# Kernel tuning notes

Hardware: AMD Instinct MI355X
Metric: run time of the kernel (lower is better)

## Reference

```python
import jax, jax.numpy as jnp
import numpy as np

H = 16  # num_heads


def setup_inputs() -> dict:
    key = jax.random.key(0)
    ks = jax.random.split(key, 12)
    B, T, D, E = 2, 2048, 1024, 16384
    s = 0.02
    return {
        "x": jax.random.normal(ks[0], (B, T, D), jnp.float32),
        "Wq": jax.random.normal(ks[1], (D, D), jnp.float32) * s,
        "bq": jnp.zeros((D,), jnp.float32),
        "Wk": jax.random.normal(ks[2], (D, D), jnp.float32) * s,
        "bk": jnp.zeros((D,), jnp.float32),
        "Wv": jax.random.normal(ks[3], (D, D), jnp.float32) * s,
        "bv": jnp.zeros((D,), jnp.float32),
        "Wo": jax.random.normal(ks[4], (D, D), jnp.float32) * s,
        "bo": jnp.zeros((D,), jnp.float32),
        "edge_emb": jax.random.normal(ks[5], (3, D), jnp.float32) * s,  # TypedEdgeEmbedding table
        "type_w": jax.random.normal(ks[6], (D,), jnp.float32) * s,      # type_to_bias Linear(D,1,bias=False)
        "edge_src": jax.random.randint(ks[7], (E,), 0, T, jnp.int32),
        "edge_dst": jax.random.randint(ks[8], (E,), 0, T, jnp.int32),
        "edge_types": jax.random.randint(ks[9], (E,), 0, 3, jnp.int32),
    }


def reference(x, Wq, bq, Wk, bk, Wv, bv, Wo, bo, edge_emb, type_w,
              edge_src, edge_dst, edge_types):
    B, T, D = x.shape
    hd = D // H
    scale = 1.0 / jnp.sqrt(jnp.float32(hd))
    # QKV projections -> [B, H, T, hd]
    q = (x @ Wq + bq).reshape(B, T, H, hd).transpose(0, 2, 1, 3)
    k = (x @ Wk + bk).reshape(B, T, H, hd).transpose(0, 2, 1, 3)
    v = (x @ Wv + bv).reshape(B, T, H, hd).transpose(0, 2, 1, 3)
    # dense attention scores [B, H, T, T]
    scores = jnp.einsum('bhqd,bhkd->bhqk', q, k) * scale
    # typed edge bias: emb lookup -> linear to scalar per edge; same across B, H
    bias_e = edge_emb[edge_types] @ type_w  # [E]
    # scatter-add bias into scores at (src, dst) for every batch/head
    scores = scores.at[:, :, edge_src, edge_dst].add(bias_e)
    attn = jax.nn.softmax(scores, axis=-1)  # dropout is identity in eval / p=0
    out = jnp.einsum('bhqk,bhkd->bhqd', attn, v)
    out = out.transpose(0, 2, 1, 3).reshape(B, T, D)
    return out @ Wo + bo
```

## Files before the change

### kernel.cpp

```cpp
#include <hip/hip_runtime.h>


typedef __attribute__((ext_vector_type(4))) float f32x4;
typedef __attribute__((ext_vector_type(16))) float f32x16;
typedef __bf16 bf16x8 __attribute__((ext_vector_type(8)));

#define DEV static __device__ __forceinline__

DEV ushort f2bf(float f) {
  unsigned u = __float_as_uint(f);
  unsigned r = u + 0x7fffu + ((u >> 16) & 1u);
  return (ushort)(r >> 16);
}

DEV float bf2f(ushort u) { return __uint_as_float((unsigned)u << 16); }

DEV void gl_lds16(const void* g, void* l) {
  __builtin_amdgcn_global_load_lds(
      (const __attribute__((address_space(1))) void*)g,
      (__attribute__((address_space(3))) void*)l, 16, 0, 0);
}

DEV f32x16 mfma32(bf16x8 a, bf16x8 b, f32x16 c) {
  return __builtin_amdgcn_mfma_f32_32x32x16_bf16(a, b, c, 0, 0, 0);
}

DEV unsigned cvtpk(float a, float b) {
  unsigned r;
  asm("v_cvt_pk_bf16_f32 %0, %1, %2" : "=v"(r) : "v"(a), "v"(b));
  return r;
}

__global__ __launch_bounds__(256) void tcvt5_kernel(
    const float* __restrict__ W0, const float* __restrict__ W1,
    const float* __restrict__ W2, const float* __restrict__ W3,
    ushort* __restrict__ Wt, const float* __restrict__ X,
    ushort* __restrict__ Y) {
  const int z = blockIdx.z;
  if (z == 4) {
    const int lb = blockIdx.y * 32 + blockIdx.x;
#pragma unroll
    for (int j = 0; j < 4; ++j) {
      const int i = lb * 1024 + j * 256 + threadIdx.x;
      float4 v = ((const float4*)X)[i];
      ushort4 o;
      o.x = f2bf(v.x); o.y = f2bf(v.y); o.z = f2bf(v.z); o.w = f2bf(v.w);
      ((ushort4*)Y)[i] = o;
    }
    return;
  }
  __shared__ float tile[32][33];
  const float* W = (z == 0) ? W0 : (z == 1) ? W1 : (z == 2) ? W2 : W3;
  ushort* dst = Wt + (size_t)z * 1048576;
  int bx = blockIdx.x * 32, by = blockIdx.y * 32;
  int tx = threadIdx.x & 31, ty = threadIdx.x >> 5;
#pragma unroll
  for (int i = 0; i < 32; i += 8)
    tile[ty + i][tx] = W[(size_t)(by + ty + i) * 1024 + bx + tx];
  __syncthreads();
#pragma unroll
  for (int i = 0; i < 32; i += 8)
    dst[(size_t)(bx + ty + i) * 1024 + by + tx] = f2bf(tile[tx][ty + i]);
}

__global__ __launch_bounds__(256) void zeroE_kernel(
    const int* __restrict__ src, const int* __restrict__ dst,
    float* __restrict__ BiasT, int E) {
  int e = blockIdx.x * 256 + threadIdx.x;
  if (e < E) BiasT[(size_t)dst[e] * 2048 + src[e]] = 0.0f;
}

__global__ __launch_bounds__(256) void scatterT2_kernel(
    const int* __restrict__ src, const int* __restrict__ dst,
    const int* __restrict__ typ, const float* __restrict__ emb,
    const float* __restrict__ tw, float* __restrict__ BiasT, int E) {
  __shared__ float red[256][3];
  const int t = threadIdx.x;
  float p0 = 0.f, p1 = 0.f, p2 = 0.f;
  for (int d = t; d < 1024; d += 256) {
    const float w = tw[d];
    p0 += emb[d] * w;
    p1 += emb[1024 + d] * w;
    p2 += emb[2048 + d] * w;
  }
  red[t][0] = p0; red[t][1] = p1; red[t][2] = p2;
  __syncthreads();
  for (int s = 128; s > 0; s >>= 1) {
    if (t < s) {
      red[t][0] += red[t + s][0];
      red[t][1] += red[t + s][1];
      red[t][2] += red[t + s][2];
    }
    __syncthreads();
  }
  int e = blockIdx.x * 256 + t;
  if (e < E) {
    const float b = red[0][typ[e]];
    atomicAdd(&BiasT[(size_t)dst[e] * 2048 + src[e]], b);
  }
}

__global__ __launch_bounds__(256) void dexpE_kernel(
    const int* __restrict__ src, const int* __restrict__ dst,
    const float* __restrict__ BiasT, ushort* __restrict__ DT4, int E) {
  int e = blockIdx.x * 256 + threadIdx.x;
  if (e < E) {
    const int k = dst[e], q = src[e];
    const float b = BiasT[(size_t)k * 2048 + q];
    DT4[((size_t)(k >> 2) * 2048 + q) * 4 + (k & 3)] = f2bf(__expf(b) - 1.0f);
  }
}

__global__ __launch_bounds__(512, 4) void gemm_qkv_kernel(
    const ushort* __restrict__ A, const ushort* __restrict__ Bt3,
    const float* __restrict__ bq, const float* __restrict__ bk,
    const float* __restrict__ bv, ushort* __restrict__ Qo,
    ushort* __restrict__ Ko, ushort* __restrict__ Vt2) {
  __shared__ alignas(16) char Als[2][16384];
  __shared__ alignas(16) char Bls[2][16384];
  const int tid = threadIdx.x, w = tid >> 6, l = tid & 63;
  const int m0 = blockIdx.y * 128, n0 = blockIdx.x * 128;
  const int sr = l >> 2, sg = l & 3;
  const int c = l & 15, gg = l >> 4;
  const int wr = (w >> 1) * 32, wc = (w & 1) * 64;

  f32x4 acc[2][4];
  const f32x4 zf = {0.f, 0.f, 0.f, 0.f};
#pragma unroll
  for (int a2 = 0; a2 < 2; ++a2)
#pragma unroll
    for (int b2 = 0; b2 < 4; ++b2) acc[a2][b2] = zf;

  auto STAGE = [&](int buf, int k0) {
#pragma unroll
    for (int j = 0; j < 2; ++j) {
      const int idx = w * 2 + j, kk = idx >> 3, mb = idx & 7;
      gl_lds16(A + (size_t)(m0 + mb * 16 + sr) * 1024 + k0 + kk * 32 + sg * 8,
               &Als[buf][idx * 1024]);
      gl_lds16(Bt3 + (size_t)(n0 + mb * 16 + sr) * 1024 + k0 + kk * 32 + sg * 8,
               &Bls[buf][idx * 1024]);
    }
  };

  STAGE(0, 0);
  STAGE(1, 64);
  for (int t = 0; t < 16; ++t) {
    const int cur = t & 1;
    if (t < 15) asm volatile("s_waitcnt vmcnt(4)" ::: "memory");
    else        asm volatile("s_waitcnt vmcnt(0)" ::: "memory");
    __builtin_amdgcn_s_barrier();

    bf16x8 af[2][2], bfr[2][4];
#pragma unroll
    for (int kk = 0; kk < 2; ++kk) {
#pragma unroll
      for (int f = 0; f < 2; ++f)
        af[kk][f] = *(const bf16x8*)&Als[cur][(kk * 8 + (wr >> 4) + f) * 1024 + c * 64 + gg * 16];
#pragma unroll
      for (int f = 0; f < 4; ++f)
        bfr[kk][f] = *(const bf16x8*)&Bls[cur][(kk * 8 + (wc >> 4) + f) * 1024 + c * 64 + gg * 16];
    }
    asm volatile("s_waitcnt lgkmcnt(0)" ::: "memory");
    __builtin_amdgcn_sched_barrier(0);
    __builtin_amdgcn_s_barrier();

    if (t < 14) STAGE(cur, (t + 2) * 64);

#pragma unroll
    for (int kk = 0; kk < 2; ++kk)
#pragma unroll
      for (int mf = 0; mf < 2; ++mf)
#pragma unroll
        for (int nf = 0; nf < 4; ++nf)
          acc[mf][nf] = __builtin_amdgcn_mfma_f32_16x16x32_bf16(
              af[kk][mf], bfr[kk][nf], acc[mf][nf], 0, 0, 0);
  }

  const int which = n0 >> 10;
  const float scale = (which == 0) ? 0.125f : 1.0f;
  const float* bias = (which == 0) ? bq : (which == 1) ? bk : bv;
#pragma unroll
  for (int mf = 0; mf < 2; ++mf) {
#pragma unroll
    for (int nf = 0; nf < 4; ++nf) {
      const int coln = (n0 & 1023) + wc + nf * 16 + c;
      const float bvv = bias[coln];
      const int h = coln >> 6, d = coln & 63;
#pragma unroll
      for (int i = 0; i < 4; ++i) {
        const int row = m0 + wr + mf * 16 + gg * 4 + i;
        const int b = row >> 11, t = row & 2047;
        const float v = (acc[mf][nf][i] + bvv) * scale;
        const ushort bfv = f2bf(v);
        if (which == 0)
          Qo[((size_t)(b * 16 + h) * 2048 + t) * 64 + d] = bfv;
        else if (which == 1)
          Ko[((size_t)(b * 16 + h) * 2048 + t) * 64 + d] = bfv;
        else
          Vt2[(((size_t)(b * 16 + h) * 32 + (t >> 6)) * 64 + d) * 64 + (t & 63)] = bfv;
      }
    }
  }
}

__global__ __launch_bounds__(256) void gemm_out_kernel(
    const ushort* __restrict__ A, const ushort* __restrict__ Bt,
    const float* __restrict__ bias, float* __restrict__ outp) {
  __shared__ alignas(16) char Als[8192];
  __shared__ alignas(16) char Bls[16384];
  const int tid = threadIdx.x, w = tid >> 6, l = tid & 63;
  const int lin = blockIdx.x;
  const int swz = (lin & 7) * 64 + (lin >> 3);
  const int m0 = (swz >> 3) * 64, n0 = (swz & 7) * 128;
  const int sr = l >> 2, sg = l & 3;
  const int c = l & 15, gg = l >> 4;
  const int wr = (w & 1) * 32, wc = (w >> 1) * 64;

  f32x4 acc[2][4];
  const f32x4 zf = {0.f, 0.f, 0.f, 0.f};
#pragma unroll
  for (int a2 = 0; a2 < 2; ++a2)
#pragma unroll
    for (int b2 = 0; b2 < 4; ++b2) acc[a2][b2] = zf;

  for (int k0 = 0; k0 < 1024; k0 += 64) {
#pragma unroll
    for (int j = 0; j < 2; ++j) {
      const int idx = w * 2 + j, kk = idx >> 2, mb = idx & 3;
      gl_lds16(A + (size_t)(m0 + mb * 16 + sr) * 1024 + k0 + kk * 32 + sg * 8,
               &Als[idx * 1024]);
    }
#pragma unroll
    for (int j = 0; j < 4; ++j) {
      const int idx = w * 4 + j, kk = idx >> 3, mb = idx & 7;
      gl_lds16(Bt + (size_t)(n0 + mb * 16 + sr) * 1024 + k0 + kk * 32 + sg * 8,
               &Bls[idx * 1024]);
    }
    __syncthreads();
#pragma unroll
    for (int kk = 0; kk < 2; ++kk) {
      bf16x8 af[2], bfr[4];
#pragma unroll
      for (int f = 0; f < 2; ++f)
        af[f] = *(const bf16x8*)&Als[(kk * 4 + (wr >> 4) + f) * 1024 + c * 64 + gg * 16];
#pragma unroll
      for (int f = 0; f < 4; ++f)
        bfr[f] = *(const bf16x8*)&Bls[(kk * 8 + (wc >> 4) + f) * 1024 + c * 64 + gg * 16];
#pragma unroll
      for (int mf = 0; mf < 2; ++mf)
#pragma unroll
        for (int nf = 0; nf < 4; ++nf)
          acc[mf][nf] = __builtin_amdgcn_mfma_f32_16x16x32_bf16(
              af[mf], bfr[nf], acc[mf][nf], 0, 0, 0);
    }
    __syncthreads();
  }

#pragma unroll
  for (int mf = 0; mf < 2; ++mf) {
#pragma unroll
    for (int nf = 0; nf < 4; ++nf) {
      const int col = n0 + wc + nf * 16 + c;
      const float bvv = bias[col];
#pragma unroll
      for (int i = 0; i < 4; ++i) {
        const int row = m0 + wr + mf * 16 + gg * 4 + i;
        outp[(size_t)row * 1024 + col] = acc[mf][nf][i] + bvv;
      }
    }
  }
}

__global__ __launch_bounds__(512, 4) void attn12_kernel(
    const ushort* __restrict__ Q, const ushort* __restrict__ K,
    const ushort* __restrict__ Vt2, const ushort* __restrict__ DT4,
    ushort* __restrict__ Out) {
  __shared__ alignas(16) char smem[65536];
  const int tid = threadIdx.x, w = tid >> 6, l = tid & 63;
  const int c = l & 31, hi = l >> 5;
  const int bid = blockIdx.x;
  const int bh = (bid & 7) * 4 + ((bid >> 3) & 3);
  const int qt = bid >> 5;
  const int bI = bh >> 4, h = bh & 15;
  const int qd = w >> 2, ww = w & 3;
  const int qw = qt * 128 + ww * 32;
  const int kq = qd * 1024;
  const int qsb = qd * 32768;
  const char* Kg = (const char*)(K + (size_t)bh * 2048 * 64);
  const char* Vg = (const char*)(Vt2 + (size_t)bh * 32 * 64 * 64);

  const ushort* Qp = Q + ((size_t)bh * 2048 + qw + c) * 64 + hi * 8;
  bf16x8 Qf[4];
#pragma unroll
  for (int ds = 0; ds < 4; ++ds) Qf[ds] = *(const bf16x8*)(Qp + ds * 16);

  const int srb = ww * 8 + (l >> 3);
  const int scol = ((l & 7) << 4) ^ ((l >> 3) << 4);
  const int cx = (c & 7) << 4;

  const ushort* Dbase = DT4 + ((size_t)(kq >> 2) * 2048 + qw + c) * 4;

  f32x16 oacc0 = {0,0,0,0,0,0,0,0,0,0,0,0,0,0,0,0};
  f32x16 oacc1 = {0,0,0,0,0,0,0,0,0,0,0,0,0,0,0,0};
  float l_run = 0.f;

  auto STAGE = [&](int buf, int t0) {
#pragma unroll
    for (int j = 0; j < 2; ++j) {
      const int r = j * 32 + srb;
      gl_lds16(Kg + (size_t)(kq + t0 + r) * 128 + scol,
               &smem[qsb + buf * 8192 + j * 4096 + ww * 1024]);
      gl_lds16(Vg + ((size_t)((kq + t0) >> 6) * 64 + r) * 128 + scol,
               &smem[qsb + 16384 + buf * 8192 + j * 4096 + ww * 1024]);
    }
  };

  STAGE(0, 0);
  for (int t = 0; t < 16; ++t) {
    const int cur = t & 1;
    __syncthreads();
    if (t < 15) STAGE(cur ^ 1, (t + 1) * 64);
    const char* KsC = smem + qsb + cur * 8192;
    const char* VsC = smem + qsb + 16384 + cur * 8192;

    f32x16 s0 = {0,0,0,0,0,0,0,0,0,0,0,0,0,0,0,0};
    f32x16 s1 = {0,0,0,0,0,0,0,0,0,0,0,0,0,0,0,0};
#pragma unroll
    for (int ds = 0; ds < 4; ++ds) {
      const int col = (ds * 32 + hi * 16) ^ cx;
      bf16x8 k0 = *(const bf16x8*)(KsC + c * 128 + col);
      bf16x8 k1 = *(const bf16x8*)(KsC + (32 + c) * 128 + col);
      s0 = mfma32(k0, Qf[ds], s0);
      s1 = mfma32(k1, Qf[ds], s1);
    }

    const ushort* dp = Dbase + (size_t)t * 16 * 8192;
    ushort4 dreg[8];
#pragma unroll
    for (int g = 0; g < 4; ++g) {
      dreg[g]     = *(const ushort4*)(dp + (size_t)(2 * g + hi) * 8192);
      dreg[4 + g] = *(const ushort4*)(dp + (size_t)(8 + 2 * g + hi) * 8192);
    }

    float ps[16];
#pragma unroll
    for (int r = 0; r < 16; ++r) {
      const float d0 = bf2f(((const ushort*)&dreg[r >> 2])[r & 3]);
      const float d1 = bf2f(((const ushort*)&dreg[4 + (r >> 2)])[r & 3]);
      float p0 = __expf(s0[r] - 3.0f);
      float p1 = __expf(s1[r] - 3.0f);
      p0 = fmaf(p0, d0, p0);
      p1 = fmaf(p1, d1, p1);
      s0[r] = p0; s1[r] = p1;
      ps[r] = p0 + p1;
    }
#pragma unroll
    for (int off = 8; off; off >>= 1)
#pragma unroll
      for (int r = 0; r < off; ++r) ps[r] += ps[r + off];
    l_run += ps[0];

    bf16x8 paf[2][2];
#pragma unroll
    for (int kt = 0; kt < 2; ++kt) {
      const f32x16& sv = kt ? s1 : s0;
#pragma unroll
      for (int sl = 0; sl < 2; ++sl) {
        const int rb = sl * 8;
        unsigned u0 = cvtpk(sv[rb + 0], sv[rb + 1]);
        unsigned u1 = cvtpk(sv[rb + 2], sv[rb + 3]);
        unsigned u2 = cvtpk(sv[rb + 4], sv[rb + 5]);
        unsigned u3 = cvtpk(sv[rb + 6], sv[rb + 7]);
        asm("v_permlane32_swap_b32 %0, %1" : "+v"(u0), "+v"(u2));
        asm("v_permlane32_swap_b32 %0, %1" : "+v"(u1), "+v"(u3));
        uint4 uu = {u0, u1, u2, u3};
        paf[kt][sl] = *(bf16x8*)&uu;
      }
    }

#pragma unroll
    for (int kt = 0; kt < 2; ++kt)
#pragma unroll
      for (int sl = 0; sl < 2; ++sl) {
        const int ks = kt * 2 + sl;
        const int col = (ks * 32 + hi * 16) ^ cx;
        bf16x8 v0 = *(const bf16x8*)(VsC + c * 128 + col);
        bf16x8 v1 = *(const bf16x8*)(VsC + (32 + c) * 128 + col);
        oacc0 = mfma32(paf[kt][sl], v0, oacc0);
        oacc1 = mfma32(paf[kt][sl], v1, oacc1);
      }
  }

  __syncthreads();
  const float l_tot = l_run + __shfl_xor(l_run, 32);
  float* mb  = (float*)smem + ww * 2048;
  float* lb  = (float*)(smem + 32768);
  float* lb2 = (float*)(smem + 32768 + 512);
  if (qd == 1) {
#pragma unroll
    for (int r = 0; r < 16; ++r) {
      const int qr = (r & 3) + 8 * (r >> 2) + 4 * hi;
      mb[qr * 64 + c] = oacc0[r];
      mb[qr * 64 + 32 + c] = oacc1[r];
    }
    lb[ww * 32 + c] = l_tot;
  }
  __syncthreads();
  if (qd == 0) {
    const float linv = 1.0f / (l_tot + lb[ww * 32 + c]);
    lb2[ww * 32 + c] = linv;
    const float* lp = lb2 + ww * 32 + hi * 4;
    f32x4 lv[4];
#pragma unroll
    for (int g2 = 0; g2 < 4; ++g2) lv[g2] = *(const f32x4*)(lp + 8 * g2);
    ushort* Ob = Out + ((size_t)bI * 2048 + qw) * 1024 + h * 64;
#pragma unroll
    for (int r = 0; r < 16; ++r) {
      const int qr = (r & 3) + 8 * (r >> 2) + 4 * hi;
      const float sc = lv[r >> 2][r & 3];
      const float o0 = (oacc0[r] + mb[qr * 64 + c]) * sc;
      const float o1 = (oacc1[r] + mb[qr * 64 + 32 + c]) * sc;
      Ob[(size_t)qr * 1024 + c] = f2bf(o0);
      Ob[(size_t)qr * 1024 + 32 + c] = f2bf(o1);
    }
  }
}

extern "C" void kernel_launch(void* const* d_in, const int* in_sizes, int n_in,
                              void* d_out, int out_size, void* d_ws, size_t ws_size,
                              hipStream_t stream) {
  (void)n_in; (void)out_size; (void)ws_size;
  const float* x   = (const float*)d_in[0];
  const float* Wq  = (const float*)d_in[1];
  const float* bq  = (const float*)d_in[2];
  const float* Wk  = (const float*)d_in[3];
  const float* bk  = (const float*)d_in[4];
  const float* Wv  = (const float*)d_in[5];
  const float* bv  = (const float*)d_in[6];
  const float* Wo  = (const float*)d_in[7];
  const float* bo  = (const float*)d_in[8];
  const float* emb = (const float*)d_in[9];
  const float* tw  = (const float*)d_in[10];
  const int* esrc  = (const int*)d_in[11];
  const int* edst  = (const int*)d_in[12];
  const int* etyp  = (const int*)d_in[13];
  const int E = in_sizes[11];

  char* ws = (char*)d_ws;
  const size_t MB = 1u << 20;
  ushort* Wtq = (ushort*)(ws + 0 * MB);
  ushort* Wto = (ushort*)(ws + 6 * MB);
  ushort* Wt3 = Wtq;
  ushort* Qb  = (ushort*)(ws + 8 * MB);
  ushort* Kb  = (ushort*)(ws + 16 * MB);
  ushort* Vt2 = (ushort*)(ws + 24 * MB);
  ushort* Ab  = (ushort*)(ws + 32 * MB);
  float*  BiasT = (float*)(ws + 40 * MB);
  ushort* xbf = (ushort*)d_out;
  ushort* DT4 = (ushort*)((char*)d_out + 8388608);

  const int eb = (E + 255) / 256;
  dim3 tg(32, 32, 5);
  tcvt5_kernel<<<tg, 256, 0, stream>>>(Wq, Wk, Wv, Wo, Wtq, x, xbf);
  (void)hipMemsetAsync(DT4, 0, (size_t)2048 * 2048 * 2, stream);
  zeroE_kernel<<<eb, 256, 0, stream>>>(esrc, edst, BiasT, E);
  scatterT2_kernel<<<eb, 256, 0, stream>>>(esrc, edst, etyp, emb, tw, BiasT, E);
  dexpE_kernel<<<eb, 256, 0, stream>>>(esrc, edst, BiasT, DT4, E);

  dim3 gqkv(24, 32);
  gemm_qkv_kernel<<<gqkv, 512, 0, stream>>>(xbf, Wt3, bq, bk, bv, Qb, Kb, Vt2);
  attn12_kernel<<<512, 512, 0, stream>>>(Qb, Kb, Vt2, DT4, Ab);
  gemm_out_kernel<<<512, 256, 0, stream>>>(Ab, Wto, bo, (float*)d_out);
}
```

Before: 147.2 us.

## Double-buffer LDS staging in output projection GEMM

Turns the output GEMM's K loop into a two-stage pipeline. Global-to-LDS loads for tile t+2 are issued into the freed buffer while MFMAs run on register fragments already read from LDS, with explicit vmcnt/lgkmcnt waits and barriers. The aim is to hide global load latency behind compute. LDS use doubles, and the launch bounds now ask for 4 blocks per CU. This only touches the smaller output projection, so its share of total time limits the effect.

```diff
diff --git a/kernel.cpp b/kernel.cpp
--- a/kernel.cpp
+++ b/kernel.cpp
@@ -203,11 +203,11 @@
   }
 }
 
-__global__ __launch_bounds__(256) void gemm_out_kernel(
+__global__ __launch_bounds__(256, 4) void gemm_out_kernel(
     const ushort* __restrict__ A, const ushort* __restrict__ Bt,
     const float* __restrict__ bias, float* __restrict__ outp) {
-  __shared__ alignas(16) char Als[8192];
-  __shared__ alignas(16) char Bls[16384];
+  __shared__ alignas(16) char Als[2][8192];
+  __shared__ alignas(16) char Bls[2][16384];
   const int tid = threadIdx.x, w = tid >> 6, l = tid & 63;
   const int lin = blockIdx.x;
   const int swz = (lin & 7) * 64 + (lin >> 3);
@@ -223,37 +223,53 @@
 #pragma unroll
     for (int b2 = 0; b2 < 4; ++b2) acc[a2][b2] = zf;
 
-  for (int k0 = 0; k0 < 1024; k0 += 64) {
+  auto STAGE = [&](int buf, int k0) {
 #pragma unroll
     for (int j = 0; j < 2; ++j) {
       const int idx = w * 2 + j, kk = idx >> 2, mb = idx & 3;
       gl_lds16(A + (size_t)(m0 + mb * 16 + sr) * 1024 + k0 + kk * 32 + sg * 8,
-               &Als[idx * 1024]);
+               &Als[buf][idx * 1024]);
     }
 #pragma unroll
     for (int j = 0; j < 4; ++j) {
       const int idx = w * 4 + j, kk = idx >> 3, mb = idx & 7;
       gl_lds16(Bt + (size_t)(n0 + mb * 16 + sr) * 1024 + k0 + kk * 32 + sg * 8,
-               &Bls[idx * 1024]);
-    }
-    __syncthreads();
+               &Bls[buf][idx * 1024]);
+    }
+  };
+
+  STAGE(0, 0);
+  STAGE(1, 64);
+  for (int t = 0; t < 16; ++t) {
+    const int cur = t & 1;
+    if (t < 15) asm volatile("s_waitcnt vmcnt(6)" ::: "memory");
+    else        asm volatile("s_waitcnt vmcnt(0)" ::: "memory");
+    __builtin_amdgcn_s_barrier();
+
+    bf16x8 af[2][2], bfr[2][4];
 #pragma unroll
     for (int kk = 0; kk < 2; ++kk) {
-      bf16x8 af[2], bfr[4];
 #pragma unroll
       for (int f = 0; f < 2; ++f)
-        af[f] = *(const bf16x8*)&Als[(kk * 4 + (wr >> 4) + f) * 1024 + c * 64 + gg * 16];
+        af[kk][f] = *(const bf16x8*)&Als[cur][(kk * 4 + (wr >> 4) + f) * 1024 + c * 64 + gg * 16];
 #pragma unroll
       for (int f = 0; f < 4; ++f)
-        bfr[f] = *(const bf16x8*)&Bls[(kk * 8 + (wc >> 4) + f) * 1024 + c * 64 + gg * 16];
+        bfr[kk][f] = *(const bf16x8*)&Bls[cur][(kk * 8 + (wc >> 4) + f) * 1024 + c * 64 + gg * 16];
+    }
+    asm volatile("s_waitcnt lgkmcnt(0)" ::: "memory");
+    __builtin_amdgcn_sched_barrier(0);
+    __builtin_amdgcn_s_barrier();
+
+    if (t < 14) STAGE(cur, (t + 2) * 64);
+
+#pragma unroll
+    for (int kk = 0; kk < 2; ++kk)
 #pragma unroll
       for (int mf = 0; mf < 2; ++mf)
 #pragma unroll
         for (int nf = 0; nf < 4; ++nf)
           acc[mf][nf] = __builtin_amdgcn_mfma_f32_16x16x32_bf16(
-              af[mf], bfr[nf], acc[mf][nf], 0, 0, 0);
-    }
-    __syncthreads();
+              af[kk][mf], bfr[kk][nf], acc[mf][nf], 0, 0, 0);
   }
 
 #pragma unroll
```

Result: no change. 148.5 us (+0.9%).
